# Optimization experiments

Hardware: AMD Instinct MI355X
Metric: run time of the kernel (lower is better)

The kernel has to match this reference:

```python
import jax, jax.numpy as jnp
import numpy as np

N = 100000   # nodes
E = 1600000  # edges (avg degree 16)
D = 128      # hidden_dim


def setup_inputs() -> dict:
    key = jax.random.key(0)
    k1, k2, k3, k4, k5, k6 = jax.random.split(key, 6)
    return {
        "t": jnp.zeros((), dtype=jnp.float32),  # unused by the ODE func
        "x": jax.random.normal(k1, (N, D), dtype=jnp.float32),
        "x0": jax.random.normal(k2, (N, D), dtype=jnp.float32),
        "alpha_train": jax.random.normal(k3, (N,), dtype=jnp.float32),
        "adj_values": jax.random.uniform(k4, (E,), dtype=jnp.float32),
        "adj_row": jax.random.randint(k5, (E,), 0, N, dtype=jnp.int32),
        "adj_col": jax.random.randint(k6, (E,), 0, N, dtype=jnp.int32),
    }


def reference(t, x, x0, alpha_train, adj_values, adj_row, adj_col):
    # alph = sigmoid(alpha_train).unsqueeze(1)  -> [N, 1]
    alph = jax.nn.sigmoid(alpha_train)[:, None]
    # ax = spmm(adj, x): COO gather of source-node features, scale by edge
    # value, scatter-add into destination rows. [N, D]
    ax = jax.ops.segment_sum(adj_values[:, None] * x[adj_col], adj_row,
                             num_segments=x.shape[0])
    # f = alph * 0.5 * (ax - x) + x0
    return alph * 0.5 * (ax - x) + x0
```

## Files before the change

kernel.cpp:

```cpp
#include <hip/hip_runtime.h>


#define DIM 128
#define RPB 64
#define RSHIFT 6
#define ACHUNK 4096
#define BCAP 2048
#define NBMAX 2048
#define HISTB 128

__device__ __forceinline__ float sigmoidf_(float a) {
    return 1.0f / (1.0f + __expf(-a));
}
__device__ __forceinline__ unsigned f2bf(float f) {
    unsigned u = __float_as_uint(f);
    return (u + 0x7FFFu + ((u >> 16) & 1u)) >> 16;
}

__global__ __launch_bounds__(256)
void xcast_hist_kernel(const float* __restrict__ x,
                       unsigned short* __restrict__ xb, int n4,
                       const int* __restrict__ row, int* __restrict__ bhist,
                       int n_edges, int nb, int xg) {
    __shared__ int h[NBMAX];
    if ((int)blockIdx.x < xg) {
        int i = blockIdx.x * 256 + threadIdx.x;
        if (i >= n4) return;
        float4 v = reinterpret_cast<const float4*>(x)[i];
        uint2 o;
        o.x = f2bf(v.x) | (f2bf(v.y) << 16);
        o.y = f2bf(v.z) | (f2bf(v.w) << 16);
        reinterpret_cast<uint2*>(xb)[i] = o;
        return;
    }
    int t = threadIdx.x;
    int bid = blockIdx.x - xg;
    for (int i = t; i < NBMAX; i += 256) h[i] = 0;
    __syncthreads();
    int e4 = n_edges >> 2;
    for (int i = bid * 256 + t; i < e4; i += HISTB * 256) {
        int4 r = reinterpret_cast<const int4*>(row)[i];
        atomicAdd(&h[r.x >> RSHIFT], 1);
        atomicAdd(&h[r.y >> RSHIFT], 1);
        atomicAdd(&h[r.z >> RSHIFT], 1);
        atomicAdd(&h[r.w >> RSHIFT], 1);
    }
    if (bid == 0 && t == 0) {
        for (int i = e4 << 2; i < n_edges; ++i)
            atomicAdd(&bhist[row[i] >> RSHIFT], 1);
    }
    __syncthreads();
    for (int i = t; i < NBMAX; i += 256)
        if (h[i]) atomicAdd(&bhist[i], h[i]);
}

__global__ __launch_bounds__(1024)
void bucket_scan_kernel(const int* __restrict__ bhist, int* __restrict__ boffs,
                        int* __restrict__ bcur, int nb) {
    __shared__ int ts[1024];
    int t = threadIdx.x;
    int i0 = 2 * t, i1 = 2 * t + 1;
    int v0 = (i0 < nb) ? bhist[i0] : 0;
    int v1 = (i1 < nb) ? bhist[i1] : 0;
    ts[t] = v0 + v1;
    __syncthreads();
    for (int off = 1; off < 1024; off <<= 1) {
        int u = (t >= off) ? ts[t - off] : 0;
        __syncthreads();
        ts[t] += u;
        __syncthreads();
    }
    int ex = (t == 0) ? 0 : ts[t - 1];
    if (i0 < nb) { boffs[i0] = ex;      bcur[i0] = ex; }
    if (i1 < nb) { boffs[i1] = ex + v0; bcur[i1] = ex + v0; }
    if (t == 1023) boffs[nb] = ts[1023];
}

__global__ __launch_bounds__(256)
void bin_kernel(const int* __restrict__ row, const int* __restrict__ col,
                const float* __restrict__ vals, int* __restrict__ bcursor,
                int2* __restrict__ epackA, int n_edges, int nb) {
    __shared__ int hist[NBMAX];
    __shared__ int lbase[NBMAX];
    __shared__ int gbase[NBMAX];
    __shared__ int lcur[NBMAX];
    __shared__ int ts[256];
    __shared__ int2 stage[ACHUNK];
    __shared__ unsigned short bkid[ACHUNK];
    int t = threadIdx.x;
    int base = blockIdx.x * ACHUNK;
    int m = n_edges - base;
    if (m > ACHUNK) m = ACHUNK;
    for (int i = t; i < NBMAX; i += 256) hist[i] = 0;
    __syncthreads();
    for (int i = t; i < m; i += 256)
        atomicAdd(&hist[row[base + i] >> RSHIFT], 1);
    __syncthreads();
    int tb = t * 8;
    int hh[8];
    int run = 0;
#pragma unroll
    for (int j = 0; j < 8; ++j) { hh[j] = hist[tb + j]; run += hh[j]; }
    ts[t] = run;
    __syncthreads();
    for (int off = 1; off < 256; off <<= 1) {
        int u = (t >= off) ? ts[t - off] : 0;
        __syncthreads();
        ts[t] += u;
        __syncthreads();
    }
    int ex = (t == 0) ? 0 : ts[t - 1];
#pragma unroll
    for (int j = 0; j < 8; ++j) { lbase[tb + j] = ex; ex += hh[j]; }
    __syncthreads();
    for (int i = t; i < nb; i += 256) {
        gbase[i] = atomicAdd(&bcursor[i], hist[i]);
        lcur[i] = 0;
    }
    __syncthreads();
    for (int i = t; i < m; i += 256) {
        int r = row[base + i];
        int c = col[base + i];
        float v = vals[base + i];
        int bk = r >> RSHIFT;
        int lp = atomicAdd(&lcur[bk], 1);
        int sp = lbase[bk] + lp;
        stage[sp] = make_int2(((r & (RPB - 1)) << 17) | c, __float_as_int(v));
        bkid[sp] = (unsigned short)bk;
    }
    __syncthreads();
    for (int i = t; i < m; i += 256) {
        int bk = bkid[i];
        epackA[gbase[bk] + (i - lbase[bk])] = stage[i];
    }
}

template <int USE_BF16>
__global__ __launch_bounds__(512)
void fused_sort_gather_kernel(const unsigned short* __restrict__ xb,
                              const float* __restrict__ x,
                              const float* __restrict__ x0,
                              const float* __restrict__ alpha,
                              const int* __restrict__ boffs,
                              const int2* __restrict__ epackA,
                              float* __restrict__ out, int n_nodes) {
    __shared__ int2 eout[BCAP];
    __shared__ int rowstart[RPB];
    __shared__ int rowcur[RPB];
    __shared__ float sval[RPB];
    int b = blockIdx.x, t = threadIdx.x;
    int r0 = b * RPB;
    int begin = boffs[b], end = boffs[b + 1];
    int n = end - begin;
    if (t < RPB) {
        int r = r0 + t;
        sval[t] = (r < n_nodes) ? 0.5f * sigmoidf_(alpha[r]) : 0.f;
        rowstart[t] = 0;
    }
    __syncthreads();
    int wave = t >> 6, lane = t & 63;
    const unsigned* xbp = reinterpret_cast<const unsigned*>(xb);
    const float2* xp = reinterpret_cast<const float2*>(x);
    if (n <= BCAP) {
        for (int i = t; i < n; i += 512)
            atomicAdd(&rowstart[epackA[begin + i].x >> 17], 1);
        __syncthreads();
        if (t < RPB) rowcur[t] = rowstart[t];
        __syncthreads();
        for (int off = 1; off < RPB; off <<= 1) {
            int u = (t < RPB && t >= off) ? rowcur[t - off] : 0;
            __syncthreads();
            if (t < RPB) rowcur[t] += u;
            __syncthreads();
        }
        if (t < RPB) {
            int excl = rowcur[t] - rowstart[t];
            rowstart[t] = excl;
            rowcur[t] = excl;
        }
        __syncthreads();
        for (int i = t; i < n; i += 512) {
            int2 e = epackA[begin + i];
            int pos = atomicAdd(&rowcur[e.x >> 17], 1);
            eout[pos] = make_int2(e.x & 0x1FFFF, e.y);
        }
        __syncthreads();
        for (int q = 0; q < 8; ++q) {
            int lr = wave * 8 + q;
            int r = r0 + lr;
            if (r >= n_nodes) break;
            float s = sval[lr];
            int rb = r * 64;
            float2 acc = reinterpret_cast<const float2*>(x0)[rb + lane];
            if (USE_BF16) {
                unsigned dx = xbp[rb + lane];
                acc.x -= s * __uint_as_float((dx & 0xFFFFu) << 16);
                acc.y -= s * __uint_as_float(dx & 0xFFFF0000u);
            } else {
                float2 xv = xp[rb + lane];
                acc.x -= s * xv.x;
                acc.y -= s * xv.y;
            }
            int k = rowstart[lr];
            int stop = (lr + 1 < RPB) ? rowstart[lr + 1] : n;
            for (; k + 8 <= stop; k += 8) {
                float w[8];
                if (USE_BF16) {
                    unsigned d[8];
#pragma unroll
                    for (int j = 0; j < 8; ++j) {
                        int2 e = eout[k + j];
                        w[j] = s * __int_as_float(e.y);
                        d[j] = xbp[(size_t)e.x * 64 + lane];
                    }
#pragma unroll
                    for (int j = 0; j < 8; ++j) {
                        acc.x += w[j] * __uint_as_float((d[j] & 0xFFFFu) << 16);
                        acc.y += w[j] * __uint_as_float(d[j] & 0xFFFF0000u);
                    }
                } else {
                    float2 v[8];
#pragma unroll
                    for (int j = 0; j < 8; ++j) {
                        int2 e = eout[k + j];
                        w[j] = s * __int_as_float(e.y);
                        v[j] = xp[(size_t)e.x * 64 + lane];
                    }
#pragma unroll
                    for (int j = 0; j < 8; ++j) {
                        acc.x += w[j] * v[j].x;
                        acc.y += w[j] * v[j].y;
                    }
                }
            }
            for (; k < stop; ++k) {
                int2 e = eout[k];
                float w = s * __int_as_float(e.y);
                if (USE_BF16) {
                    unsigned d = xbp[(size_t)e.x * 64 + lane];
                    acc.x += w * __uint_as_float((d & 0xFFFFu) << 16);
                    acc.y += w * __uint_as_float(d & 0xFFFF0000u);
                } else {
                    float2 v = xp[(size_t)e.x * 64 + lane];
                    acc.x += w * v.x;
                    acc.y += w * v.y;
                }
            }
            reinterpret_cast<float2*>(out)[rb + lane] = acc;
        }
    } else {
        for (int q = 0; q < 8; ++q) {
            int lr = wave * 8 + q;
            int r = r0 + lr;
            if (r >= n_nodes) break;
            float s = sval[lr];
            int rb = r * 64;
            float2 acc = reinterpret_cast<const float2*>(x0)[rb + lane];
            if (USE_BF16) {
                unsigned dx = xbp[rb + lane];
                acc.x -= s * __uint_as_float((dx & 0xFFFFu) << 16);
                acc.y -= s * __uint_as_float(dx & 0xFFFF0000u);
            } else {
                float2 xv = xp[rb + lane];
                acc.x -= s * xv.x;
                acc.y -= s * xv.y;
            }
            for (int i = 0; i < n; ++i) {
                int2 e = epackA[begin + i];
                if ((e.x >> 17) == lr) {
                    float w = s * __int_as_float(e.y);
                    if (USE_BF16) {
                        unsigned d = xbp[(size_t)(e.x & 0x1FFFF) * 64 + lane];
                        acc.x += w * __uint_as_float((d & 0xFFFFu) << 16);
                        acc.y += w * __uint_as_float(d & 0xFFFF0000u);
                    } else {
                        float2 v = xp[(size_t)(e.x & 0x1FFFF) * 64 + lane];
                        acc.x += w * v.x;
                        acc.y += w * v.y;
                    }
                }
            }
            reinterpret_cast<float2*>(out)[rb + lane] = acc;
        }
    }
}

extern "C" void kernel_launch(void* const* d_in, const int* in_sizes, int n_in,
                              void* d_out, int out_size, void* d_ws, size_t ws_size,
                              hipStream_t stream) {
    const float* x     = (const float*)d_in[1];
    const float* x0    = (const float*)d_in[2];
    const float* alpha = (const float*)d_in[3];
    const float* vals  = (const float*)d_in[4];
    const int*   row   = (const int*)d_in[5];
    const int*   col   = (const int*)d_in[6];
    float* out = (float*)d_out;

    int n_nodes = in_sizes[3];
    int n_edges = in_sizes[4];
    int nb = (n_nodes + RPB - 1) / RPB;

    size_t xb_bytes = (size_t)n_nodes * DIM * sizeof(unsigned short);
    size_t ep_bytes = (size_t)((n_edges + 3) & ~3) * sizeof(int2);
    size_t meta_bytes = (size_t)(NBMAX + NBMAX + 16 + NBMAX) * sizeof(int);
    int use_bf16 = (ws_size >= xb_bytes + ep_bytes + meta_bytes + 512) ? 1 : 0;

    unsigned short* xxb;
    int2* epackA;
    int* bhist;
    if (use_bf16) {
        xxb    = (unsigned short*)d_ws;
        epackA = (int2*)((char*)d_ws + xb_bytes);
        bhist  = (int*)((char*)epackA + ep_bytes);
    } else {
        xxb    = nullptr;
        epackA = (int2*)d_ws;
        bhist  = (int*)((char*)epackA + ep_bytes);
    }
    int* boffs = bhist + NBMAX;
    int* bcur  = boffs + NBMAX + 16;

    hipMemsetAsync(bhist, 0, NBMAX * sizeof(int), stream);

    {
        int n4 = use_bf16 ? ((n_nodes * DIM) >> 2) : 0;
        int xg = use_bf16 ? ((n4 + 255) / 256) : 0;
        xcast_hist_kernel<<<xg + HISTB, 256, 0, stream>>>(
            x, xxb, n4, row, bhist, n_edges, nb, xg);
    }
    bucket_scan_kernel<<<1, 1024, 0, stream>>>(bhist, boffs, bcur, nb);
    {
        int grid = (n_edges + ACHUNK - 1) / ACHUNK;
        bin_kernel<<<grid, 256, 0, stream>>>(row, col, vals, bcur, epackA,
                                             n_edges, nb);
    }
    if (use_bf16) {
        fused_sort_gather_kernel<1><<<nb, 512, 0, stream>>>(
            xxb, x, x0, alpha, boffs, epackA, out, n_nodes);
    } else {
        fused_sort_gather_kernel<0><<<nb, 512, 0, stream>>>(
            xxb, x, x0, alpha, boffs, epackA, out, n_nodes);
    }
}
```

Baseline: 134.6 us.

## Fold bucket scan into bin kernel, halve chunk size, use nontemporal x0/out access

Removes the separate single-block bucket_scan kernel. Each bin_kernel block now redundantly scans the global bucket histogram itself, block 0 writes boffs, and the global cursor becomes a zero-initialised relative counter added to the scanned base. ACHUNK is halved so there are more, smaller binning blocks with less shared memory each. The gather kernel loads x0 and stores out with nontemporal hints to avoid polluting cache needed by the gathered x rows. The trade-off is redundant per-block scan work and extra barriers in exchange for one fewer launch and serial dependency.

```diff
diff --git a/kernel.cpp b/kernel.cpp
--- a/kernel.cpp
+++ b/kernel.cpp
@@ -4,10 +4,12 @@
 #define DIM 128
 #define RPB 64
 #define RSHIFT 6
-#define ACHUNK 4096
+#define ACHUNK 2048
 #define BCAP 2048
 #define NBMAX 2048
 #define HISTB 128
+
+typedef float f2v __attribute__((ext_vector_type(2)));
 
 __device__ __forceinline__ float sigmoidf_(float a) {
     return 1.0f / (1.0f + __expf(-a));
@@ -54,36 +56,16 @@
         if (h[i]) atomicAdd(&bhist[i], h[i]);
 }
 
-__global__ __launch_bounds__(1024)
-void bucket_scan_kernel(const int* __restrict__ bhist, int* __restrict__ boffs,
-                        int* __restrict__ bcur, int nb) {
-    __shared__ int ts[1024];
-    int t = threadIdx.x;
-    int i0 = 2 * t, i1 = 2 * t + 1;
-    int v0 = (i0 < nb) ? bhist[i0] : 0;
-    int v1 = (i1 < nb) ? bhist[i1] : 0;
-    ts[t] = v0 + v1;
-    __syncthreads();
-    for (int off = 1; off < 1024; off <<= 1) {
-        int u = (t >= off) ? ts[t - off] : 0;
-        __syncthreads();
-        ts[t] += u;
-        __syncthreads();
-    }
-    int ex = (t == 0) ? 0 : ts[t - 1];
-    if (i0 < nb) { boffs[i0] = ex;      bcur[i0] = ex; }
-    if (i1 < nb) { boffs[i1] = ex + v0; bcur[i1] = ex + v0; }
-    if (t == 1023) boffs[nb] = ts[1023];
-}
-
 __global__ __launch_bounds__(256)
 void bin_kernel(const int* __restrict__ row, const int* __restrict__ col,
-                const float* __restrict__ vals, int* __restrict__ bcursor,
+                const float* __restrict__ vals,
+                const int* __restrict__ bhist, int* __restrict__ gcur,
+                int* __restrict__ boffs,
                 int2* __restrict__ epackA, int n_edges, int nb) {
     __shared__ int hist[NBMAX];
     __shared__ int lbase[NBMAX];
     __shared__ int gbase[NBMAX];
-    __shared__ int lcur[NBMAX];
+    __shared__ int SH[NBMAX];
     __shared__ int ts[256];
     __shared__ int2 stage[ACHUNK];
     __shared__ unsigned short bkid[ACHUNK];
@@ -95,13 +77,12 @@
     __syncthreads();
     for (int i = t; i < m; i += 256)
         atomicAdd(&hist[row[base + i] >> RSHIFT], 1);
-    __syncthreads();
     int tb = t * 8;
-    int hh[8];
-    int run = 0;
-#pragma unroll
-    for (int j = 0; j < 8; ++j) { hh[j] = hist[tb + j]; run += hh[j]; }
-    ts[t] = run;
+    int gh[8];
+    int grun = 0;
+#pragma unroll
+    for (int j = 0; j < 8; ++j) { gh[j] = bhist[tb + j]; grun += gh[j]; }
+    ts[t] = grun;
     __syncthreads();
     for (int off = 1; off < 256; off <<= 1) {
         int u = (t >= off) ? ts[t - off] : 0;
@@ -109,21 +90,47 @@
         ts[t] += u;
         __syncthreads();
     }
-    int ex = (t == 0) ? 0 : ts[t - 1];
-#pragma unroll
-    for (int j = 0; j < 8; ++j) { lbase[tb + j] = ex; ex += hh[j]; }
+    {
+        int ex = (t == 0) ? 0 : ts[t - 1];
+#pragma unroll
+        for (int j = 0; j < 8; ++j) { SH[tb + j] = ex; ex += gh[j]; }
+    }
+    __syncthreads();
+    if (blockIdx.x == 0) {
+        for (int i = t; i <= nb; i += 256)
+            boffs[i] = (i < NBMAX) ? SH[i] : n_edges;
+    }
+    int lh[8];
+    int lrun = 0;
+#pragma unroll
+    for (int j = 0; j < 8; ++j) { lh[j] = hist[tb + j]; lrun += lh[j]; }
+    ts[t] = lrun;
+    __syncthreads();
+    for (int off = 1; off < 256; off <<= 1) {
+        int u = (t >= off) ? ts[t - off] : 0;
+        __syncthreads();
+        ts[t] += u;
+        __syncthreads();
+    }
+    {
+        int ex = (t == 0) ? 0 : ts[t - 1];
+#pragma unroll
+        for (int j = 0; j < 8; ++j) { lbase[tb + j] = ex; ex += lh[j]; }
+    }
     __syncthreads();
     for (int i = t; i < nb; i += 256) {
-        gbase[i] = atomicAdd(&bcursor[i], hist[i]);
-        lcur[i] = 0;
-    }
+        int hv = hist[i];
+        gbase[i] = SH[i] + (hv ? atomicAdd(&gcur[i], hv) : 0);
+    }
+    __syncthreads();
+    for (int i = t; i < NBMAX; i += 256) SH[i] = 0;
     __syncthreads();
     for (int i = t; i < m; i += 256) {
         int r = row[base + i];
         int c = col[base + i];
         float v = vals[base + i];
         int bk = r >> RSHIFT;
-        int lp = atomicAdd(&lcur[bk], 1);
+        int lp = atomicAdd(&SH[bk], 1);
         int sp = lbase[bk] + lp;
         stage[sp] = make_int2(((r & (RPB - 1)) << 17) | c, __float_as_int(v));
         bkid[sp] = (unsigned short)bk;
@@ -161,6 +168,8 @@
     int wave = t >> 6, lane = t & 63;
     const unsigned* xbp = reinterpret_cast<const unsigned*>(xb);
     const float2* xp = reinterpret_cast<const float2*>(x);
+    const f2v* x0v = reinterpret_cast<const f2v*>(x0);
+    f2v* outv = reinterpret_cast<f2v*>(out);
     if (n <= BCAP) {
         for (int i = t; i < n; i += 512)
             atomicAdd(&rowstart[epackA[begin + i].x >> 17], 1);
@@ -191,7 +200,8 @@
             if (r >= n_nodes) break;
             float s = sval[lr];
             int rb = r * 64;
-            float2 acc = reinterpret_cast<const float2*>(x0)[rb + lane];
+            f2v a0 = __builtin_nontemporal_load(&x0v[rb + lane]);
+            float2 acc = make_float2(a0.x, a0.y);
             if (USE_BF16) {
                 unsigned dx = xbp[rb + lane];
                 acc.x -= s * __uint_as_float((dx & 0xFFFFu) << 16);
@@ -246,7 +256,8 @@
                     acc.y += w * v.y;
                 }
             }
-            reinterpret_cast<float2*>(out)[rb + lane] = acc;
+            f2v o; o.x = acc.x; o.y = acc.y;
+            __builtin_nontemporal_store(o, &outv[rb + lane]);
         }
     } else {
         for (int q = 0; q < 8; ++q) {
@@ -302,7 +313,7 @@
 
     size_t xb_bytes = (size_t)n_nodes * DIM * sizeof(unsigned short);
     size_t ep_bytes = (size_t)((n_edges + 3) & ~3) * sizeof(int2);
-    size_t meta_bytes = (size_t)(NBMAX + NBMAX + 16 + NBMAX) * sizeof(int);
+    size_t meta_bytes = (size_t)(NBMAX + NBMAX + NBMAX + 16) * sizeof(int);
     int use_bf16 = (ws_size >= xb_bytes + ep_bytes + meta_bytes + 512) ? 1 : 0;
 
     unsigned short* xxb;
@@ -317,10 +328,10 @@
         epackA = (int2*)d_ws;
         bhist  = (int*)((char*)epackA + ep_bytes);
     }
-    int* boffs = bhist + NBMAX;
-    int* bcur  = boffs + NBMAX + 16;
-
-    hipMemsetAsync(bhist, 0, NBMAX * sizeof(int), stream);
+    int* gcur  = bhist + NBMAX;
+    int* boffs = gcur + NBMAX;
+
+    hipMemsetAsync(bhist, 0, 2 * NBMAX * sizeof(int), stream);
 
     {
         int n4 = use_bf16 ? ((n_nodes * DIM) >> 2) : 0;
@@ -328,11 +339,10 @@
         xcast_hist_kernel<<<xg + HISTB, 256, 0, stream>>>(
             x, xxb, n4, row, bhist, n_edges, nb, xg);
     }
-    bucket_scan_kernel<<<1, 1024, 0, stream>>>(bhist, boffs, bcur, nb);
     {
         int grid = (n_edges + ACHUNK - 1) / ACHUNK;
-        bin_kernel<<<grid, 256, 0, stream>>>(row, col, vals, bcur, epackA,
-                                             n_edges, nb);
+        bin_kernel<<<grid, 256, 0, stream>>>(row, col, vals, bhist, gcur,
+                                             boffs, epackA, n_edges, nb);
     }
     if (use_bf16) {
         fused_sort_gather_kernel<1><<<nb, 512, 0, stream>>>(
```

Result: slower. 150.1 us (+11.6%).
